# Kernel optimization log

Hardware: AMD Instinct MI355X
Metric: run time of the kernel (lower is better)

Reference implementation:

```python
import math
import jax, jax.numpy as jnp
import numpy as np

EPS = 1e-12
NHEAD = 12
HEAD_DIM = 64  # d_model // nhead = 768 // 12


def setup_inputs() -> dict:
    key = jax.random.key(0)
    ks = jax.random.split(key, 8)
    L, D, H = 12, 768, 2048
    B, S = 8, 1024
    std = 0.02
    return {
        "x": jax.random.normal(ks[0], (B, S, D), jnp.float32),
        "wq": jax.random.normal(ks[1], (L, D, D), jnp.float32) * std,
        "wk": jax.random.normal(ks[2], (L, D, D), jnp.float32) * std,
        "wv": jax.random.normal(ks[3], (L, D, D), jnp.float32) * std,
        "wo": jax.random.normal(ks[4], (L, D, D), jnp.float32) * std,
        "w1": jax.random.normal(ks[5], (L, H, D), jnp.float32) * std,
        "w2": jax.random.normal(ks[6], (L, D, H), jnp.float32) * std,
        "attn_norm_w": jnp.ones((L, D), jnp.float32),
        "ffn_norm_w": jnp.ones((L, D), jnp.float32),
    }


def _rmsnorm(x, w):
    # x * rsqrt(mean(x^2) + eps) * w
    return x * jax.lax.rsqrt(jnp.mean(x * x, axis=-1, keepdims=True) + EPS) * w


def _block(x, params):
    wq, wk, wv, wo, w1, w2, anw, fnw = params
    B, S, D = x.shape
    # --- attention (manual matmul-softmax-matmul, fp32 softmax) ---
    xn = _rmsnorm(x, anw)
    q = jnp.einsum('bsd,ed->bse', xn, wq).reshape(B, S, NHEAD, HEAD_DIM)
    k = jnp.einsum('bsd,ed->bse', xn, wk).reshape(B, S, NHEAD, HEAD_DIM)
    v = jnp.einsum('bsd,ed->bse', xn, wv).reshape(B, S, NHEAD, HEAD_DIM)
    scores = jnp.einsum('bqhd,bkhd->bhqk', q, k) / math.sqrt(HEAD_DIM)
    probs = jax.nn.softmax(scores.astype(jnp.float32), axis=-1).astype(x.dtype)
    attn = jnp.einsum('bhqk,bkhd->bqhd', probs, v).reshape(B, S, D)
    h = x + jnp.einsum('bsd,ed->bse', attn, wo)
    # --- FFN: w2(silu(w1(h_norm))) ---
    hn = _rmsnorm(h, fnw)
    ff = jnp.einsum('bsh,dh->bsd', jax.nn.silu(jnp.einsum('bsd,hd->bsh', hn, w1)), w2)
    return h + ff


def reference(x, wq, wk, wv, wo, w1, w2, attn_norm_w, ffn_norm_w):
    def step(carry, p):
        return _block(carry, p), None
    out, _ = jax.lax.scan(step, x, (wq, wk, wv, wo, w1, w2, attn_norm_w, ffn_norm_w))
    return out
```

## Files before the change

### kernel.cpp

```cpp
#include <hip/hip_runtime.h>
#include <stdint.h>

typedef unsigned short u16;
typedef unsigned int u32;
typedef __bf16 bf16x8 __attribute__((ext_vector_type(8)));
typedef __bf16 bf16x4 __attribute__((ext_vector_type(4)));
typedef float f32x4 __attribute__((ext_vector_type(4)));

__device__ __forceinline__ u16 f2bf(float f) {
  u32 u = __builtin_bit_cast(u32, f);
  u32 r = (u + 0x7FFFu + ((u >> 16) & 1u)) >> 16;
  return (u16)r;
}

__global__ __launch_bounds__(256)
void convert_w(const float* __restrict__ wq, const float* __restrict__ wk,
               const float* __restrict__ wv, const float* __restrict__ wo,
               const float* __restrict__ w1, const float* __restrict__ w2,
               u16* __restrict__ out) {
  size_t i = ((size_t)blockIdx.x * 256 + threadIdx.x) * 4;
  if (i >= 5505024) return;
  const float* src; size_t off;
  if (i < 589824)       { src = wq; off = i; }
  else if (i < 1179648) { src = wk; off = i - 589824; }
  else if (i < 1769472) { src = wv; off = i - 1179648; }
  else if (i < 2359296) { src = wo; off = i - 1769472; }
  else if (i < 3932160) { src = w1; off = i - 2359296; }
  else                  { src = w2; off = i - 3932160; }
  float4 v = *(const float4*)(src + off);
  u32 lo = (u32)f2bf(v.x) | ((u32)f2bf(v.y) << 16);
  u32 hi = (u32)f2bf(v.z) | ((u32)f2bf(v.w) << 16);
  *(uint2*)(out + i) = make_uint2(lo, hi);
}

__device__ __forceinline__ void rn_store4(u16* p, float4 v, float4 w, float sc) {
  u32 lo = (u32)f2bf(v.x * sc * w.x) | ((u32)f2bf(v.y * sc * w.y) << 16);
  u32 hi = (u32)f2bf(v.z * sc * w.z) | ((u32)f2bf(v.w * sc * w.w) << 16);
  *(uint2*)p = make_uint2(lo, hi);
}

__global__ __launch_bounds__(256)
void rmsnorm_k(const float* __restrict__ x, const float* __restrict__ w,
               u16* __restrict__ out) {
  const int tok = (blockIdx.x << 2) + (threadIdx.x >> 6);
  const int l = threadIdx.x & 63;
  const float* xr = x + (size_t)tok * 768;
  float4 v0 = *(const float4*)(xr + l * 4);
  float4 v1 = *(const float4*)(xr + 256 + l * 4);
  float4 v2 = *(const float4*)(xr + 512 + l * 4);
  float ss = v0.x*v0.x + v0.y*v0.y + v0.z*v0.z + v0.w*v0.w
           + v1.x*v1.x + v1.y*v1.y + v1.z*v1.z + v1.w*v1.w
           + v2.x*v2.x + v2.y*v2.y + v2.z*v2.z + v2.w*v2.w;
  ss += __shfl_xor(ss, 1);  ss += __shfl_xor(ss, 2);  ss += __shfl_xor(ss, 4);
  ss += __shfl_xor(ss, 8);  ss += __shfl_xor(ss, 16); ss += __shfl_xor(ss, 32);
  float sc = rsqrtf(ss * (1.f / 768.f) + 1e-12f);
  float4 w0 = *(const float4*)(w + l * 4);
  float4 w1v = *(const float4*)(w + 256 + l * 4);
  float4 w2v = *(const float4*)(w + 512 + l * 4);
  u16* o = out + (size_t)tok * 768;
  rn_store4(o + l * 4, v0, w0, sc);
  rn_store4(o + 256 + l * 4, v1, w1v, sc);
  rn_store4(o + 512 + l * 4, v2, w2v, sc);
}

#define GEMM_CORE(A_, W_, K_, m0_, n0_)                                             \
  for (int kt = 0; kt < (K_); kt += 64) {                                           \
    __syncthreads();                                                                \
    _Pragma("unroll")                                                               \
    for (int ii = 0; ii < 4; ++ii) {                                                \
      int issue = (w << 2) + ii;                                                    \
      int r = (issue << 3) + (l >> 3);                                              \
      int c = (l & 7) ^ (r & 7);                                                    \
      __builtin_amdgcn_global_load_lds((A_) + (size_t)((m0_) + r) * (K_) + kt + c * 8, \
                                       As + issue * 512, 16, 0, 0);                 \
      __builtin_amdgcn_global_load_lds((W_) + (size_t)((n0_) + r) * (K_) + kt + c * 8, \
                                       Ws + issue * 512, 16, 0, 0);                 \
    }                                                                               \
    __syncthreads();                                                                \
    _Pragma("unroll")                                                               \
    for (int kc = 0; kc < 2; ++kc) {                                                \
      int chunk = lg + (kc << 2);                                                   \
      bf16x8 af[4], bfr[4];                                                         \
      _Pragma("unroll")                                                             \
      for (int i = 0; i < 4; ++i) {                                                 \
        int mr = (wm << 6) + (i << 4) + ll;                                         \
        af[i] = *(const bf16x8*)((const char*)As + mr * 128 + ((chunk ^ (mr & 7)) << 4)); \
        int nr = (wn << 6) + (i << 4) + ll;                                         \
        bfr[i] = *(const bf16x8*)((const char*)Ws + nr * 128 + ((chunk ^ (nr & 7)) << 4)); \
      }                                                                             \
      _Pragma("unroll")                                                             \
      for (int i = 0; i < 4; ++i)                                                   \
        _Pragma("unroll")                                                           \
        for (int j = 0; j < 4; ++j)                                                 \
          acc[i][j] = __builtin_amdgcn_mfma_f32_16x16x32_bf16(af[i], bfr[j], acc[i][j], 0, 0, 0); \
    }                                                                               \
  }

template<int EP>
__global__ __launch_bounds__(256, 2)
void gemm_bt(const u16* __restrict__ A, const u16* __restrict__ W,
             void* __restrict__ outp, const float* __restrict__ Res,
             int M, int N, int K) {
  __shared__ __align__(16) u16 As[128 * 64];
  __shared__ __align__(16) u16 Ws[128 * 64];
  const int tid = threadIdx.x;
  const int w = tid >> 6, l = tid & 63;
  const int lg = l >> 4, ll = l & 15;
  const int ntiles = N >> 7;
  const int mt = blockIdx.x / ntiles, nt = blockIdx.x - mt * ntiles;
  const int m0 = mt << 7, n0 = nt << 7;
  const int wm = w >> 1, wn = w & 1;

  const f32x4 fz = {0.f, 0.f, 0.f, 0.f};
  f32x4 acc[4][4];
#pragma unroll
  for (int i = 0; i < 4; ++i)
#pragma unroll
    for (int j = 0; j < 4; ++j) acc[i][j] = fz;

  GEMM_CORE(A, W, K, m0, n0)

  const int g4 = lg << 2;
#pragma unroll
  for (int i = 0; i < 4; ++i) {
#pragma unroll
    for (int j = 0; j < 4; ++j) {
      int row0 = m0 + (wm << 6) + (i << 4) + g4;
      int col = n0 + (wn << 6) + (j << 4) + ll;
      f32x4 v = acc[i][j];
      if (EP == 0) {
        u16* o = (u16*)outp;
#pragma unroll
        for (int e = 0; e < 4; ++e) o[(size_t)(row0 + e) * N + col] = f2bf(v[e]);
      } else if (EP == 1) {
        float* o = (float*)outp;
#pragma unroll
        for (int e = 0; e < 4; ++e) {
          size_t idx = (size_t)(row0 + e) * N + col;
          o[idx] = Res[idx] + v[e];
        }
      } else {
        u16* o = (u16*)outp;
#pragma unroll
        for (int e = 0; e < 4; ++e) {
          float xx = v[e];
          o[(size_t)(row0 + e) * N + col] = f2bf(xx / (1.f + __expf(-xx)));
        }
      }
    }
  }
}

__global__ __launch_bounds__(256, 4)
void gemm_bt64(const u16* __restrict__ A, const u16* __restrict__ W,
               float* __restrict__ outp, const float* __restrict__ Res,
               int M, int N, int K) {
  __shared__ __align__(16) u16 As[64 * 64];
  __shared__ __align__(16) u16 Ws[128 * 64];
  const int tid = threadIdx.x;
  const int w = tid >> 6, l = tid & 63;
  const int lg = l >> 4, ll = l & 15;
  const int ntiles = N >> 7;
  const int mt = blockIdx.x / ntiles, nt = blockIdx.x - mt * ntiles;
  const int m0 = mt << 6, n0 = nt << 7;
  const int wm = w >> 1, wn = w & 1;

  const f32x4 fz = {0.f, 0.f, 0.f, 0.f};
  f32x4 acc[2][4];
#pragma unroll
  for (int i = 0; i < 2; ++i)
#pragma unroll
    for (int j = 0; j < 4; ++j) acc[i][j] = fz;

  for (int kt = 0; kt < K; kt += 64) {
    __syncthreads();
#pragma unroll
    for (int ii = 0; ii < 6; ++ii) {
      int issue = w * 6 + ii;
      if (issue < 8) {
        int r = (issue << 3) + (l >> 3);
        int c = (l & 7) ^ (r & 7);
        __builtin_amdgcn_global_load_lds(A + (size_t)(m0 + r) * K + kt + c * 8,
                                         As + issue * 512, 16, 0, 0);
      } else {
        int is2 = issue - 8;
        int r = (is2 << 3) + (l >> 3);
        int c = (l & 7) ^ (r & 7);
        __builtin_amdgcn_global_load_lds(W + (size_t)(n0 + r) * K + kt + c * 8,
                                         Ws + is2 * 512, 16, 0, 0);
      }
    }
    __syncthreads();
#pragma unroll
    for (int kc = 0; kc < 2; ++kc) {
      int chunk = lg + (kc << 2);
      bf16x8 af[2], bfr[4];
#pragma unroll
      for (int i = 0; i < 2; ++i) {
        int mr = (wm << 5) + (i << 4) + ll;
        af[i] = *(const bf16x8*)((const char*)As + mr * 128 + ((chunk ^ (mr & 7)) << 4));
      }
#pragma unroll
      for (int j = 0; j < 4; ++j) {
        int nr = (wn << 6) + (j << 4) + ll;
        bfr[j] = *(const bf16x8*)((const char*)Ws + nr * 128 + ((chunk ^ (nr & 7)) << 4));
      }
#pragma unroll
      for (int i = 0; i < 2; ++i)
#pragma unroll
        for (int j = 0; j < 4; ++j)
          acc[i][j] = __builtin_amdgcn_mfma_f32_16x16x32_bf16(af[i], bfr[j], acc[i][j], 0, 0, 0);
    }
  }

  const int g4 = lg << 2;
#pragma unroll
  for (int i = 0; i < 2; ++i) {
#pragma unroll
    for (int j = 0; j < 4; ++j) {
      int row0 = m0 + (wm << 5) + (i << 4) + g4;
      int col = n0 + (wn << 6) + (j << 4) + ll;
      f32x4 v = acc[i][j];
#pragma unroll
      for (int e = 0; e < 4; ++e) {
        size_t idx = (size_t)(row0 + e) * N + col;
        outp[idx] = Res[idx] + v[e];
      }
    }
  }
}

__global__ __launch_bounds__(256, 2)
void gemm_qkv(const u16* __restrict__ A, const u16* __restrict__ W,
              u16* __restrict__ Qo, u16* __restrict__ Ko, u16* __restrict__ Vo) {
  __shared__ __align__(16) u16 As[128 * 64];
  __shared__ __align__(16) u16 Ws[128 * 64];
  const int tid = threadIdx.x;
  const int w = tid >> 6, l = tid & 63;
  const int lg = l >> 4, ll = l & 15;
  const int mt = blockIdx.x / 18, nt = blockIdx.x - mt * 18;
  const int m0 = mt << 7, n0 = nt << 7;
  const int wm = w >> 1, wn = w & 1;
  const int K = 768;

  const f32x4 fz = {0.f, 0.f, 0.f, 0.f};
  f32x4 acc[4][4];
#pragma unroll
  for (int i = 0; i < 4; ++i)
#pragma unroll
    for (int j = 0; j < 4; ++j) acc[i][j] = fz;

  GEMM_CORE(A, W, K, m0, n0)

  const int g4 = lg << 2;
#pragma unroll
  for (int i = 0; i < 4; ++i) {
#pragma unroll
    for (int j = 0; j < 4; ++j) {
      int row0 = m0 + (wm << 6) + (i << 4) + g4;
      int col = n0 + (wn << 6) + (j << 4) + ll;
      f32x4 v = acc[i][j];
      if (nt < 12) {
        u16* o = (nt < 6) ? Qo : Ko;
        int c = (nt < 6) ? col : (col - 768);
#pragma unroll
        for (int e = 0; e < 4; ++e) o[(size_t)(row0 + e) * 768 + c] = f2bf(v[e]);
      } else {
        int c = col - 1536;
        int vrow = ((row0 >> 10) * 768) + c;
        u32 lo = (u32)f2bf(v[0]) | ((u32)f2bf(v[1]) << 16);
        u32 hi = (u32)f2bf(v[2]) | ((u32)f2bf(v[3]) << 16);
        *(uint2*)(Vo + ((size_t)vrow << 10) + (row0 & 1023)) = make_uint2(lo, hi);
      }
    }
  }
}

__global__ __launch_bounds__(256, 2)
void attn_kernel(const u16* __restrict__ Q, const u16* __restrict__ Kg,
                 const u16* __restrict__ Vt, u16* __restrict__ Og) {
  __shared__ __align__(16) u16 Ks[128 * 64];
  __shared__ __align__(16) u16 Vs[64 * 128];
  __shared__ __align__(16) __bf16 Ps[4][16 * 128];

  const int tid = threadIdx.x;
  const int w = tid >> 6, l = tid & 63;
  const int lg = l >> 4, ll = l & 15;
  const int bid = blockIdx.x;
  const int qt = bid / 96;
  const int bh = bid - qt * 96;
  const int b = bh / 12, hh = bh - b * 12;
  const float SC = 0.125f * 1.44269504f;

  bf16x8 qf[2][2];
  {
    const int tq = (b << 10) + (qt << 7) + (w << 5);
#pragma unroll
    for (int fm = 0; fm < 2; ++fm)
#pragma unroll
      for (int kc = 0; kc < 2; ++kc)
        qf[fm][kc] = *(const bf16x8*)(Q + (size_t)(tq + fm * 16 + ll) * 768 + hh * 64 + kc * 32 + lg * 8);
  }

  const f32x4 fz = {0.f, 0.f, 0.f, 0.f};
  f32x4 oacc[4][2];
#pragma unroll
  for (int i = 0; i < 4; ++i) { oacc[i][0] = fz; oacc[i][1] = fz; }
  float mrow2[2] = {-1e30f, -1e30f};
  float lrow2[2] = {0.f, 0.f};

  for (int kt = 0; kt < 8; ++kt) {
    __syncthreads();
#pragma unroll
    for (int ii = 0; ii < 4; ++ii) {
      int issue = (w << 2) + ii;
      int r = (issue << 3) + (l >> 3);
      int c = (l & 7) ^ (r & 7);
      __builtin_amdgcn_global_load_lds(
          Kg + (size_t)((b << 10) + (kt << 7) + r) * 768 + hh * 64 + c * 8,
          Ks + issue * 512, 16, 0, 0);
      int rv = (issue << 2) + (l >> 4);
      int cv = ll ^ (rv & 7);
      __builtin_amdgcn_global_load_lds(
          Vt + (size_t)((bh << 6) + rv) * 1024 + (kt << 7) + cv * 8,
          Vs + issue * 512, 16, 0, 0);
    }
    __syncthreads();

    f32x4 sa[2][8];
#pragma unroll
    for (int fm = 0; fm < 2; ++fm)
#pragma unroll
      for (int fn = 0; fn < 8; ++fn) sa[fm][fn] = fz;
#pragma unroll
    for (int kc = 0; kc < 2; ++kc) {
      int chunk = lg + (kc << 2);
      bf16x8 kb[8];
#pragma unroll
      for (int fn = 0; fn < 8; ++fn) {
        int nr = (fn << 4) + ll;
        kb[fn] = *(const bf16x8*)((const char*)Ks + nr * 128 + ((chunk ^ (nr & 7)) << 4));
      }
#pragma unroll
      for (int fm = 0; fm < 2; ++fm)
#pragma unroll
        for (int fn = 0; fn < 8; ++fn)
          sa[fm][fn] = __builtin_amdgcn_mfma_f32_16x16x32_bf16(kb[fn], qf[fm][kc], sa[fm][fn], 0, 0, 0);
    }
#pragma unroll
    for (int fm = 0; fm < 2; ++fm)
#pragma unroll
      for (int fn = 0; fn < 8; ++fn) sa[fm][fn] *= SC;

#pragma unroll
    for (int fm = 0; fm < 2; ++fm) {
      f32x4 vm = sa[fm][0];
#pragma unroll
      for (int fn = 1; fn < 8; ++fn) {
#pragma unroll
        for (int e = 0; e < 4; ++e) vm[e] = fmaxf(vm[e], sa[fm][fn][e]);
      }
      float mx = fmaxf(fmaxf(vm[0], vm[1]), fmaxf(vm[2], vm[3]));
      mx = fmaxf(mx, __shfl_xor(mx, 16));
      mx = fmaxf(mx, __shfl_xor(mx, 32));
      float mnew = fmaxf(mrow2[fm], mx);
      float scal = __builtin_amdgcn_exp2f(mrow2[fm] - mnew);

      f32x4 vsum = fz;
#pragma unroll
      for (int fn = 0; fn < 8; ++fn) {
        f32x4 p;
#pragma unroll
        for (int e = 0; e < 4; ++e) p[e] = __builtin_amdgcn_exp2f(sa[fm][fn][e] - mnew);
        vsum += p;
        bf16x4 pv4;
#pragma unroll
        for (int e = 0; e < 4; ++e) pv4[e] = (__bf16)p[e];
        int chunk = (fn << 1) + (lg >> 1);
        *(bf16x4*)((char*)&Ps[w][0] + ll * 256 + ((chunk ^ (ll & 7)) << 4) + ((lg & 1) << 3)) = pv4;
      }
      float rs = (vsum[0] + vsum[1]) + (vsum[2] + vsum[3]);
      rs += __shfl_xor(rs, 16);
      rs += __shfl_xor(rs, 32);
      lrow2[fm] = lrow2[fm] * scal + rs;
      mrow2[fm] = mnew;

      asm volatile("" ::: "memory");

#pragma unroll
      for (int fd = 0; fd < 4; ++fd) oacc[fd][fm] *= scal;

#pragma unroll
      for (int ch = 0; ch < 4; ++ch) {
        int chunk = lg + (ch << 2);
        int qr = ll;
        bf16x8 pb = *(const bf16x8*)((const char*)&Ps[w][0] + qr * 256 + ((chunk ^ (qr & 7)) << 4));
#pragma unroll
        for (int fd = 0; fd < 4; ++fd) {
          int dr = (fd << 4) + ll;
          bf16x8 av = *(const bf16x8*)((const char*)Vs + dr * 256 + ((chunk ^ (dr & 7)) << 4));
          oacc[fd][fm] = __builtin_amdgcn_mfma_f32_16x16x32_bf16(av, pb, oacc[fd][fm], 0, 0, 0);
        }
      }

      asm volatile("" ::: "memory");
    }
  }

  float inv0 = 1.f / lrow2[0];
  float inv1 = 1.f / lrow2[1];
  const int tq0 = (b << 10) + (qt << 7) + (w << 5);
#pragma unroll
  for (int fd = 0; fd < 4; ++fd) {
#pragma unroll
    for (int fo = 0; fo < 2; ++fo) {
      int q = (fo << 4) + ll;
      float inv = fo ? inv1 : inv0;
      f32x4 v = oacc[fd][fo];
      int d0 = (fd << 4) + (lg << 2);
      u16* o = Og + (size_t)(tq0 + q) * 768 + hh * 64 + d0;
      u32 lo = (u32)f2bf(v[0] * inv) | ((u32)f2bf(v[1] * inv) << 16);
      u32 hi = (u32)f2bf(v[2] * inv) | ((u32)f2bf(v[3] * inv) << 16);
      *(uint2*)o = make_uint2(lo, hi);
    }
  }
}

extern "C" void kernel_launch(void* const* d_in, const int* in_sizes, int n_in,
                              void* d_out, int out_size, void* d_ws, size_t ws_size,
                              hipStream_t stream) {
  const float* x = (const float*)d_in[0];
  const float* wq = (const float*)d_in[1];
  const float* wk = (const float*)d_in[2];
  const float* wv = (const float*)d_in[3];
  const float* wo = (const float*)d_in[4];
  const float* w1 = (const float*)d_in[5];
  const float* w2 = (const float*)d_in[6];
  const float* anw = (const float*)d_in[7];
  const float* fnw = (const float*)d_in[8];

  char* ws = (char*)d_ws;
  float* h    = (float*)(ws);
  u16* xn     = (u16*)(ws + 25165824);
  u16* qb     = (u16*)(ws + 37748736);
  u16* kb     = (u16*)(ws + 50331648);
  u16* vt     = (u16*)(ws + 62914560);
  u16* ff1    = (u16*)(ws + 75497472);
  u16* wbuf   = (u16*)(ws + 109051904);

  hipMemcpyAsync(h, x, 25165824, hipMemcpyDeviceToDevice, stream);

  for (int L = 0; L < 12; ++L) {
    convert_w<<<5376, 256, 0, stream>>>(
        wq + (size_t)L * 589824, wk + (size_t)L * 589824,
        wv + (size_t)L * 589824, wo + (size_t)L * 589824,
        w1 + (size_t)L * 1572864, w2 + (size_t)L * 1572864, wbuf);
    rmsnorm_k<<<2048, 256, 0, stream>>>(h, anw + L * 768, xn);
    gemm_qkv<<<1152, 256, 0, stream>>>(xn, wbuf, qb, kb, vt);
    attn_kernel<<<768, 256, 0, stream>>>(qb, kb, vt, qb);
    gemm_bt64<<<768, 256, 0, stream>>>(qb, wbuf + 1769472, h, h, 8192, 768, 768);
    rmsnorm_k<<<2048, 256, 0, stream>>>(h, fnw + L * 768, xn);
    gemm_bt<2><<<1024, 256, 0, stream>>>(xn, wbuf + 2359296, ff1, nullptr, 8192, 2048, 768);
    float* outw = (L == 11) ? (float*)d_out : h;
    gemm_bt64<<<768, 256, 0, stream>>>(ff1, wbuf + 3932160, outw, h, 8192, 768, 2048);
  }
}
```

Measured before the change: 2.653 ms.

## Prefetch next K/V tile into registers during attention compute

Replaces direct global-to-LDS loads with register prefetch of the next K/V tile, issued before the current tile's compute and written to LDS afterwards. This hides global load latency behind the MFMA and softmax work. It also folds the softmax scale into an FMA inside exp2 instead of a separate multiply pass, and raises wave priority around MFMA sections. The cost is extra registers for the prefetch buffers, which could limit occupancy under launch_bounds(256,2).

```diff
diff --git a/kernel.cpp b/kernel.cpp
--- a/kernel.cpp
+++ b/kernel.cpp
@@ -279,8 +279,8 @@
 __global__ __launch_bounds__(256, 2)
 void attn_kernel(const u16* __restrict__ Q, const u16* __restrict__ Kg,
                  const u16* __restrict__ Vt, u16* __restrict__ Og) {
-  __shared__ __align__(16) u16 Ks[128 * 64];
-  __shared__ __align__(16) u16 Vs[64 * 128];
+  __shared__ __align__(16) __bf16 Ks[128 * 64];
+  __shared__ __align__(16) __bf16 Vs[64 * 128];
   __shared__ __align__(16) __bf16 Ps[4][16 * 128];
 
   const int tid = threadIdx.x;
@@ -302,6 +302,26 @@
         qf[fm][kc] = *(const bf16x8*)(Q + (size_t)(tq + fm * 16 + ll) * 768 + hh * 64 + kc * 32 + lg * 8);
   }
 
+  bf16x8 kp[4], vp[4];
+#define ISSUE_KV(t_)                                                                  \
+  { _Pragma("unroll")                                                                 \
+    for (int ii = 0; ii < 4; ++ii) {                                                  \
+      int issue = (w << 2) + ii;                                                      \
+      int r = (issue << 3) + (l >> 3);                                                \
+      int c = (l & 7) ^ (r & 7);                                                      \
+      kp[ii] = *(const bf16x8*)(Kg + (size_t)((b << 10) + ((t_) << 7) + r) * 768 + hh * 64 + c * 8); \
+      int rv = (issue << 2) + (l >> 4);                                               \
+      int cv = ll ^ (rv & 7);                                                         \
+      vp[ii] = *(const bf16x8*)(Vt + (size_t)((bh << 6) + rv) * 1024 + ((t_) << 7) + cv * 8); \
+    } }
+#define WRITE_KV                                                                      \
+  { _Pragma("unroll")                                                                 \
+    for (int ii = 0; ii < 4; ++ii) {                                                  \
+      int issue = (w << 2) + ii;                                                      \
+      *(bf16x8*)((char*)Ks + issue * 1024 + l * 16) = kp[ii];                         \
+      *(bf16x8*)((char*)Vs + issue * 1024 + l * 16) = vp[ii];                         \
+    } }
+
   const f32x4 fz = {0.f, 0.f, 0.f, 0.f};
   f32x4 oacc[4][2];
 #pragma unroll
@@ -309,29 +329,19 @@
   float mrow2[2] = {-1e30f, -1e30f};
   float lrow2[2] = {0.f, 0.f};
 
+  ISSUE_KV(0);
+  WRITE_KV;
+  __syncthreads();
+
   for (int kt = 0; kt < 8; ++kt) {
-    __syncthreads();
-#pragma unroll
-    for (int ii = 0; ii < 4; ++ii) {
-      int issue = (w << 2) + ii;
-      int r = (issue << 3) + (l >> 3);
-      int c = (l & 7) ^ (r & 7);
-      __builtin_amdgcn_global_load_lds(
-          Kg + (size_t)((b << 10) + (kt << 7) + r) * 768 + hh * 64 + c * 8,
-          Ks + issue * 512, 16, 0, 0);
-      int rv = (issue << 2) + (l >> 4);
-      int cv = ll ^ (rv & 7);
-      __builtin_amdgcn_global_load_lds(
-          Vt + (size_t)((bh << 6) + rv) * 1024 + (kt << 7) + cv * 8,
-          Vs + issue * 512, 16, 0, 0);
-    }
-    __syncthreads();
+    if (kt < 7) ISSUE_KV(kt + 1);
 
     f32x4 sa[2][8];
 #pragma unroll
     for (int fm = 0; fm < 2; ++fm)
 #pragma unroll
       for (int fn = 0; fn < 8; ++fn) sa[fm][fn] = fz;
+    __builtin_amdgcn_s_setprio(1);
 #pragma unroll
     for (int kc = 0; kc < 2; ++kc) {
       int chunk = lg + (kc << 2);
@@ -347,10 +357,7 @@
         for (int fn = 0; fn < 8; ++fn)
           sa[fm][fn] = __builtin_amdgcn_mfma_f32_16x16x32_bf16(kb[fn], qf[fm][kc], sa[fm][fn], 0, 0, 0);
     }
-#pragma unroll
-    for (int fm = 0; fm < 2; ++fm)
-#pragma unroll
-      for (int fn = 0; fn < 8; ++fn) sa[fm][fn] *= SC;
+    __builtin_amdgcn_s_setprio(0);
 
 #pragma unroll
     for (int fm = 0; fm < 2; ++fm) {
@@ -364,14 +371,16 @@
       mx = fmaxf(mx, __shfl_xor(mx, 16));
       mx = fmaxf(mx, __shfl_xor(mx, 32));
       float mnew = fmaxf(mrow2[fm], mx);
-      float scal = __builtin_amdgcn_exp2f(mrow2[fm] - mnew);
+      float c2 = mnew * SC;
+      float scal = __builtin_amdgcn_exp2f(__builtin_fmaf(SC, mrow2[fm], -c2));
 
       f32x4 vsum = fz;
 #pragma unroll
       for (int fn = 0; fn < 8; ++fn) {
         f32x4 p;
 #pragma unroll
-        for (int e = 0; e < 4; ++e) p[e] = __builtin_amdgcn_exp2f(sa[fm][fn][e] - mnew);
+        for (int e = 0; e < 4; ++e)
+          p[e] = __builtin_amdgcn_exp2f(__builtin_fmaf(SC, sa[fm][fn][e], -c2));
         vsum += p;
         bf16x4 pv4;
 #pragma unroll
@@ -390,6 +399,7 @@
 #pragma unroll
       for (int fd = 0; fd < 4; ++fd) oacc[fd][fm] *= scal;
 
+      __builtin_amdgcn_s_setprio(1);
 #pragma unroll
       for (int ch = 0; ch < 4; ++ch) {
         int chunk = lg + (ch << 2);
@@ -402,10 +412,19 @@
           oacc[fd][fm] = __builtin_amdgcn_mfma_f32_16x16x32_bf16(av, pb, oacc[fd][fm], 0, 0, 0);
         }
       }
+      __builtin_amdgcn_s_setprio(0);
 
       asm volatile("" ::: "memory");
     }
-  }
+
+    if (kt < 7) {
+      __syncthreads();
+      WRITE_KV;
+      __syncthreads();
+    }
+  }
+#undef ISSUE_KV
+#undef WRITE_KV
 
   float inv0 = 1.f / lrow2[0];
   float inv1 = 1.f / lrow2[1];
```

New measurement: 2.646 ms. No clear change (-0.2%).
